# Optimization experiments

Measured on AMD Instinct MI355X. Metric: run time of the kernel, lower is better.

## Reference

```python
import jax, jax.numpy as jnp
import numpy as np

N_EXPERTS = 8
TOP_K = 2

def setup_inputs() -> dict:
    key = jax.random.key(0)
    k1, k2, k3, k4 = jax.random.split(key, 4)
    B, T, C, F, E = 4, 1024, 1024, 2048, N_EXPERTS
    x = jax.random.normal(k1, (B, T, C), dtype=jnp.float32)
    router_w = jax.random.normal(k2, (E, C), dtype=jnp.float32) * 0.02
    w_v = jax.random.normal(k3, (E, C, 2 * F), dtype=jnp.float32) * 0.02
    c_proj = jax.random.normal(k4, (E, F, C), dtype=jnp.float32) * 0.02
    return {"x": x, "router_w": router_w, "w_v": w_v, "c_proj": c_proj}

def reference(x, router_w, w_v, c_proj):
    B, T, C = x.shape
    E = router_w.shape[0]
    # Router: top-k softmax
    logits = jnp.einsum('btc,ec->bte', x, router_w)
    probs = jax.nn.softmax(logits, axis=-1)
    weights, indices = jax.lax.top_k(probs, TOP_K)          # [B,T,K]
    weights = weights / jnp.sum(weights, axis=-1, keepdims=True)
    avg_probs = jnp.mean(probs, axis=(0, 1))
    aux_loss = E * jnp.sum(avg_probs * avg_probs)
    # Dense per-expert SwiGLU MLP on all tokens (idiomatic jax MoE reference)
    xf = x.reshape(B * T, C)                                # [N,C]
    h = jnp.einsum('nc,ecf->enf', xf, w_v)                  # [E,N,2F]
    gate, value = jnp.split(h, 2, axis=-1)
    act = jax.nn.silu(gate) * value                         # [E,N,F]
    eo = jnp.einsum('enf,efc->nec', act, c_proj)            # [N,E,C]
    # Combine: gather each token's top-k expert outputs and weight-sum
    idx = indices.reshape(B * T, TOP_K)                     # [N,K]
    w = weights.reshape(B * T, TOP_K)                       # [N,K]
    sel = jnp.take_along_axis(eo, idx[:, :, None], axis=1)  # [N,K,C]
    out = jnp.sum(w[:, :, None] * sel, axis=1)              # [N,C]
    return out.reshape(B, T, C), aux_loss
```

## Files before the change

kernel.cpp:

```cpp
#include <hip/hip_runtime.h>
#include <hip/hip_bf16.h>
#include <stdint.h>

#define N_TOK 4096
#define C_DIM 1024
#define F_DIM 2048
#define E_NUM 8
#define SMAX 9216
#define TILES_MAX 72
#define RBLK 1024

typedef __attribute__((ext_vector_type(4))) float f32x4;
typedef __attribute__((ext_vector_type(8))) short s16x8;

__device__ __forceinline__ uint16_t f2bf(float f) {
    unsigned x;
    __builtin_memcpy(&x, &f, 4);
    unsigned r = (x + 0x7fffu + ((x >> 16) & 1u)) >> 16;
    return (uint16_t)r;
}
__device__ __forceinline__ float bf2f(uint16_t u) {
    unsigned v = (unsigned)u << 16;
    float f;
    __builtin_memcpy(&f, &v, 4);
    return f;
}

#define GLL16(gp, lp)                                                                  \
    __builtin_amdgcn_global_load_lds((const __attribute__((address_space(1))) unsigned int*)(gp), \
                                     (__attribute__((address_space(3))) unsigned int*)(lp), 16, 0, 0)

__global__ void router_kernel(const float* __restrict__ x, const float* __restrict__ rw,
                              int* __restrict__ topk_idx, float* __restrict__ topk_w,
                              float* __restrict__ psum_part, int* __restrict__ cnt_part) {
    __shared__ float s_p[E_NUM];
    __shared__ int s_c[E_NUM];
    if (threadIdx.x < E_NUM) { s_p[threadIdx.x] = 0.f; s_c[threadIdx.x] = 0; }
    __syncthreads();

    int lane = threadIdx.x & 63;
    int wv = threadIdx.x >> 6;
    int t = blockIdx.x * 4 + wv;

    const float* xr = x + (size_t)t * C_DIM + lane * 16;
    float xs[16];
    for (int i = 0; i < 4; i++) *(float4*)&xs[i * 4] = *(const float4*)(xr + i * 4);

    float acc[E_NUM];
    for (int e = 0; e < E_NUM; e++) {
        const float* wr = rw + e * C_DIM + lane * 16;
        float s = 0.f;
        for (int i = 0; i < 4; i++) {
            float4 v = *(const float4*)(wr + i * 4);
            s += xs[i * 4] * v.x + xs[i * 4 + 1] * v.y + xs[i * 4 + 2] * v.z + xs[i * 4 + 3] * v.w;
        }
        acc[e] = s;
    }
    for (int off = 32; off > 0; off >>= 1)
        for (int e = 0; e < E_NUM; e++) acc[e] += __shfl_down(acc[e], off, 64);

    if (lane == 0) {
        float m = acc[0];
        for (int e = 1; e < E_NUM; e++) m = fmaxf(m, acc[e]);
        float p[E_NUM], s = 0.f;
        for (int e = 0; e < E_NUM; e++) { p[e] = __expf(acc[e] - m); s += p[e]; }
        float inv = 1.f / s;
        for (int e = 0; e < E_NUM; e++) { p[e] *= inv; atomicAdd(&s_p[e], p[e]); }
        int i0 = 0;
        for (int e = 1; e < E_NUM; e++) if (p[e] > p[i0]) i0 = e;
        int i1 = (i0 == 0) ? 1 : 0;
        for (int e = 0; e < E_NUM; e++) if (e != i0 && p[e] > p[i1]) i1 = e;
        float w0 = p[i0], w1 = p[i1], wsum = w0 + w1;
        topk_idx[t * 2] = i0; topk_idx[t * 2 + 1] = i1;
        topk_w[t * 2] = w0 / wsum; topk_w[t * 2 + 1] = w1 / wsum;
        atomicAdd(&s_c[i0], 1); atomicAdd(&s_c[i1], 1);
    }
    __syncthreads();
    if (threadIdx.x < E_NUM) {
        psum_part[blockIdx.x * E_NUM + threadIdx.x] = s_p[threadIdx.x];
        cnt_part[blockIdx.x * E_NUM + threadIdx.x] = s_c[threadIdx.x];
    }
}

__global__ void reduce_plan_kernel(const float* __restrict__ psum_part, const int* __restrict__ cnt_part,
                                   int* __restrict__ offsets, int* __restrict__ tile_expert,
                                   int* __restrict__ tile_row0, float* __restrict__ aux_out) {
    __shared__ float sp[256];
    __shared__ int sc[256];
    __shared__ int s_count[E_NUM];
    __shared__ float s_psum[E_NUM];
    int e = threadIdx.x >> 5, i = threadIdx.x & 31;
    float fp = 0.f; int c = 0;
    for (int j = i; j < RBLK; j += 32) { fp += psum_part[j * E_NUM + e]; c += cnt_part[j * E_NUM + e]; }
    sp[threadIdx.x] = fp; sc[threadIdx.x] = c;
    __syncthreads();
    for (int s = 16; s > 0; s >>= 1) {
        if (i < s) { sp[threadIdx.x] += sp[threadIdx.x + s]; sc[threadIdx.x] += sc[threadIdx.x + s]; }
        __syncthreads();
    }
    if (i == 0) { s_count[e] = sc[threadIdx.x]; s_psum[e] = sp[threadIdx.x]; }
    __syncthreads();
    if (threadIdx.x == 0) {
        int off = 0, t = 0;
        for (int ee = 0; ee < E_NUM; ee++) {
            offsets[ee] = off;
            int n = s_count[ee];
            int nt = (n + 127) >> 7;
            for (int k = 0; k < nt; k++) { tile_expert[t] = ee; tile_row0[t] = off + k * 128; t++; }
            off += nt * 128;
        }
        offsets[E_NUM] = off;
        for (; t < TILES_MAX; t++) tile_expert[t] = -1;
        float s = 0.f;
        for (int ee = 0; ee < E_NUM; ee++) { float a = s_psum[ee] * (1.f / N_TOK); s += a * a; }
        aux_out[0] = 8.f * s;
    }
}

__global__ void assign_kernel(const int* __restrict__ topk_idx, const float* __restrict__ topk_w,
                              const int* __restrict__ offsets, int* __restrict__ count2,
                              int* __restrict__ slot_map, float* __restrict__ slot_w,
                              int* __restrict__ tok_slot) {
    __shared__ int h[E_NUM];
    __shared__ int base[E_NUM];
    if (threadIdx.x < E_NUM) h[threadIdx.x] = 0;
    __syncthreads();
    int item = blockIdx.x * 256 + threadIdx.x;
    int e = topk_idx[item];
    int rank = atomicAdd(&h[e], 1);
    __syncthreads();
    if (threadIdx.x < E_NUM)
        base[threadIdx.x] = offsets[threadIdx.x] + atomicAdd(&count2[threadIdx.x], h[threadIdx.x]);
    __syncthreads();
    int slot = base[e] + rank;
    slot_map[slot] = item;
    slot_w[slot] = topk_w[item];
    tok_slot[item] = slot;
}

__global__ void gather_kernel(const float* __restrict__ x, const int* __restrict__ slot_map,
                              uint16_t* __restrict__ x_slots) {
    int slot = blockIdx.x;
    int item = slot_map[slot];
    if (item < 0) return;
    int t = item >> 1;
    float4 v = *(const float4*)(x + (size_t)t * C_DIM + threadIdx.x * 4);
    union { uint16_t u[4]; uint2 q; } r;
    r.u[0] = f2bf(v.x); r.u[1] = f2bf(v.y); r.u[2] = f2bf(v.z); r.u[3] = f2bf(v.w);
    *(uint2*)(x_slots + (size_t)slot * C_DIM + threadIdx.x * 4) = r.q;
}

__global__ __launch_bounds__(256) void convT_kernel(const float* __restrict__ in,
                                                    uint16_t* __restrict__ out, int R, int Cc) {
    __shared__ uint16_t s[128 * 66];
    size_t zb = (size_t)blockIdx.z * (size_t)R * Cc;
    int c0 = blockIdx.x * 64, r0 = blockIdx.y * 128;
    int cx = (threadIdx.x & 15) * 4, ry = threadIdx.x >> 4;
    for (int j = 0; j < 8; j++) {
        int r = ry + j * 16;
        float4 v = *(const float4*)(in + zb + (size_t)(r0 + r) * Cc + c0 + cx);
        uint16_t* p = &s[r * 66 + cx];
        p[0] = f2bf(v.x); p[1] = f2bf(v.y); p[2] = f2bf(v.z); p[3] = f2bf(v.w);
    }
    __syncthreads();
    int oc = threadIdx.x & 63, wseg = threadIdx.x >> 6;
    uint16_t tmp[32];
    for (int j = 0; j < 32; j++) tmp[j] = s[(wseg * 32 + j) * 66 + oc];
    uint4* dst = (uint4*)(out + zb + (size_t)(c0 + oc) * R + r0 + wseg * 32);
    dst[0] = *(const uint4*)&tmp[0];
    dst[1] = *(const uint4*)&tmp[8];
    dst[2] = *(const uint4*)&tmp[16];
    dst[3] = *(const uint4*)&tmp[24];
}


__global__ __launch_bounds__(256) void gemm1_kernel(const uint16_t* __restrict__ x_slots,
                                                    const uint16_t* __restrict__ wvT,
                                                    const int* __restrict__ tile_expert,
                                                    const int* __restrict__ tile_row0,
                                                    uint16_t* __restrict__ act) {
    int e = tile_expert[blockIdx.y];
    if (e < 0) return;
    int row0 = tile_row0[blockIdx.y];
    int j = blockIdx.x;
    __shared__ uint16_t As[128 * 32];
    __shared__ uint16_t Bg[64 * 32];
    __shared__ uint16_t Bv[64 * 32];
    int lane = threadIdx.x & 63, w = threadIdx.x >> 6;
    int wm = w & 1, wn = w >> 1;
    const uint16_t* wvb = wvT + (size_t)e * 4096 * 1024;

    int sk = (((lane & 3) ^ ((lane >> 3) & 3))) * 8;
    int ar = w * 32 + (lane >> 2);
    const uint16_t* agp0 = x_slots + (size_t)(row0 + ar) * C_DIM + sk;
    const uint16_t* agp1 = agp0 + (size_t)16 * C_DIM;
    int br = w * 16 + (lane >> 2);
    const uint16_t* bgp = wvb + (size_t)(j * 64 + br) * C_DIM + sk;
    const uint16_t* bvp = wvb + (size_t)(2048 + j * 64 + br) * C_DIM + sk;

    int cswz = ((lane >> 4) ^ ((lane >> 1) & 3)) * 8;

    f32x4 accg[4][2], accv[4][2];
    f32x4 z4 = {0.f, 0.f, 0.f, 0.f};
    for (int mf = 0; mf < 4; mf++)
        for (int nf = 0; nf < 2; nf++) { accg[mf][nf] = z4; accv[mf][nf] = z4; }

    for (int kt = 0; kt < 32; ++kt) {
        int ko = kt * 32;
        __syncthreads();
        GLL16(agp0 + ko, As + w * 1024);
        GLL16(agp1 + ko, As + w * 1024 + 512);
        GLL16(bgp + ko, Bg + w * 512);
        GLL16(bvp + ko, Bv + w * 512);
        __syncthreads();
        s16x8 af[4], bg[2], bv[2];
        for (int mf = 0; mf < 4; mf++)
            af[mf] = *(const s16x8*)&As[(wm * 64 + mf * 16 + (lane & 15)) * 32 + cswz];
        for (int nf = 0; nf < 2; nf++) {
            bg[nf] = *(const s16x8*)&Bg[(wn * 32 + nf * 16 + (lane & 15)) * 32 + cswz];
            bv[nf] = *(const s16x8*)&Bv[(wn * 32 + nf * 16 + (lane & 15)) * 32 + cswz];
        }
        for (int mf = 0; mf < 4; mf++)
            for (int nf = 0; nf < 2; nf++) {
                accg[mf][nf] = __builtin_amdgcn_mfma_f32_16x16x32_bf16(af[mf], bg[nf], accg[mf][nf], 0, 0, 0);
                accv[mf][nf] = __builtin_amdgcn_mfma_f32_16x16x32_bf16(af[mf], bv[nf], accv[mf][nf], 0, 0, 0);
            }
    }
    for (int mf = 0; mf < 4; mf++)
        for (int nf = 0; nf < 2; nf++)
            for (int r = 0; r < 4; r++) {
                int row = row0 + wm * 64 + mf * 16 + (lane >> 4) * 4 + r;
                int col = j * 64 + wn * 32 + nf * 16 + (lane & 15);
                float g = accg[mf][nf][r], v = accv[mf][nf][r];
                float a = g * v / (1.f + __expf(-g));
                act[(size_t)row * F_DIM + col] = f2bf(a);
            }
}

__global__ __launch_bounds__(256) void gemm2_kernel(const uint16_t* __restrict__ act,
                                                    const uint16_t* __restrict__ cpT,
                                                    const int* __restrict__ tile_expert,
                                                    const int* __restrict__ tile_row0,
                                                    const int* __restrict__ slot_map,
                                                    const float* __restrict__ slot_w,
                                                    uint16_t* __restrict__ eo) {
    int e = tile_expert[blockIdx.y];
    if (e < 0) return;
    int row0 = tile_row0[blockIdx.y];
    int cb = blockIdx.x * 128;
    __shared__ uint16_t As[128 * 32];
    __shared__ uint16_t Bs[128 * 32];
    int lane = threadIdx.x & 63, w = threadIdx.x >> 6;
    int wm = w & 1, wn = w >> 1;
    const uint16_t* cpb = cpT + (size_t)e * 1024 * 2048;

    int sk = (((lane & 3) ^ ((lane >> 3) & 3))) * 8;
    int ar = w * 32 + (lane >> 2);
    const uint16_t* agp0 = act + (size_t)(row0 + ar) * F_DIM + sk;
    const uint16_t* agp1 = agp0 + (size_t)16 * F_DIM;
    const uint16_t* bgp0 = cpb + (size_t)(cb + ar) * F_DIM + sk;
    const uint16_t* bgp1 = bgp0 + (size_t)16 * F_DIM;

    int cswz = ((lane >> 4) ^ ((lane >> 1) & 3)) * 8;

    f32x4 acc[4][4];
    f32x4 z4 = {0.f, 0.f, 0.f, 0.f};
    for (int mf = 0; mf < 4; mf++)
        for (int nf = 0; nf < 4; nf++) acc[mf][nf] = z4;

    for (int kt = 0; kt < 64; ++kt) {
        int ko = kt * 32;
        __syncthreads();
        GLL16(agp0 + ko, As + w * 1024);
        GLL16(agp1 + ko, As + w * 1024 + 512);
        GLL16(bgp0 + ko, Bs + w * 1024);
        GLL16(bgp1 + ko, Bs + w * 1024 + 512);
        __syncthreads();
        s16x8 af[4], bf[4];
        for (int mf = 0; mf < 4; mf++)
            af[mf] = *(const s16x8*)&As[(wm * 64 + mf * 16 + (lane & 15)) * 32 + cswz];
        for (int nf = 0; nf < 4; nf++)
            bf[nf] = *(const s16x8*)&Bs[(wn * 64 + nf * 16 + (lane & 15)) * 32 + cswz];
        for (int mf = 0; mf < 4; mf++)
            for (int nf = 0; nf < 4; nf++)
                acc[mf][nf] = __builtin_amdgcn_mfma_f32_16x16x32_bf16(af[mf], bf[nf], acc[mf][nf], 0, 0, 0);
    }
    for (int mf = 0; mf < 4; mf++)
        for (int r = 0; r < 4; r++) {
            int slotr = row0 + wm * 64 + mf * 16 + (lane >> 4) * 4 + r;
            int t2k = slot_map[slotr];
            if (t2k < 0) continue;
            float wgt = slot_w[slotr];
            for (int nf = 0; nf < 4; nf++) {
                int col = cb + wn * 64 + nf * 16 + (lane & 15);
                eo[(size_t)slotr * C_DIM + col] = f2bf(wgt * acc[mf][nf][r]);
            }
        }
}

__global__ void combine_kernel(const uint16_t* __restrict__ eo, const int* __restrict__ tok_slot,
                               float* __restrict__ out) {
    int t = blockIdx.x;
    int s0 = tok_slot[2 * t], s1 = tok_slot[2 * t + 1];
    int c = threadIdx.x * 4;
    uint2 a = *(const uint2*)(eo + (size_t)s0 * C_DIM + c);
    uint2 b = *(const uint2*)(eo + (size_t)s1 * C_DIM + c);
    float4 o;
    o.x = bf2f((uint16_t)(a.x & 0xffff)) + bf2f((uint16_t)(b.x & 0xffff));
    o.y = bf2f((uint16_t)(a.x >> 16)) + bf2f((uint16_t)(b.x >> 16));
    o.z = bf2f((uint16_t)(a.y & 0xffff)) + bf2f((uint16_t)(b.y & 0xffff));
    o.w = bf2f((uint16_t)(a.y >> 16)) + bf2f((uint16_t)(b.y >> 16));
    *(float4*)(out + (size_t)t * C_DIM + c) = o;
}

extern "C" void kernel_launch(void* const* d_in, const int* in_sizes, int n_in,
                              void* d_out, int out_size, void* d_ws, size_t ws_size,
                              hipStream_t stream) {
    (void)in_sizes; (void)n_in; (void)out_size; (void)ws_size;
    const float* x = (const float*)d_in[0];
    const float* rw = (const float*)d_in[1];
    const float* wv = (const float*)d_in[2];
    const float* cp = (const float*)d_in[3];
    float* out = (float*)d_out;

    char* ws = (char*)d_ws;
    size_t off = 0;
    auto alloc = [&](size_t sz) -> void* {
        off = (off + 255) & ~(size_t)255;
        void* p = ws + off;
        off += sz;
        return p;
    };
    uint16_t* wvT = (uint16_t*)alloc((size_t)E_NUM * 4096 * 1024 * 2);
    uint16_t* cpT = (uint16_t*)alloc((size_t)E_NUM * 1024 * 2048 * 2);
    uint16_t* x_slots = (uint16_t*)alloc((size_t)SMAX * C_DIM * 2);
    uint16_t* act = (uint16_t*)alloc((size_t)SMAX * F_DIM * 2);
    uint16_t* eo = (uint16_t*)alloc((size_t)SMAX * C_DIM * 2);
    float* psum_part = (float*)alloc((size_t)RBLK * E_NUM * 4);
    int* cnt_part = (int*)alloc((size_t)RBLK * E_NUM * 4);
    int* count2 = (int*)alloc(E_NUM * 4);
    int* offsets = (int*)alloc((E_NUM + 1) * 4);
    int* tile_expert = (int*)alloc(TILES_MAX * 4);
    int* tile_row0 = (int*)alloc(TILES_MAX * 4);
    int* topk_idx = (int*)alloc((size_t)N_TOK * 2 * 4);
    float* topk_w = (float*)alloc((size_t)N_TOK * 2 * 4);
    int* slot_map = (int*)alloc((size_t)SMAX * 4);
    float* slot_w = (float*)alloc((size_t)SMAX * 4);
    int* tok_slot = (int*)alloc((size_t)N_TOK * 2 * 4);

    hipMemsetAsync(count2, 0, E_NUM * 4, stream);
    hipMemsetAsync(slot_map, 0xFF, (size_t)SMAX * 4, stream);

    router_kernel<<<RBLK, 256, 0, stream>>>(x, rw, topk_idx, topk_w, psum_part, cnt_part);
    reduce_plan_kernel<<<1, 256, 0, stream>>>(psum_part, cnt_part, offsets, tile_expert, tile_row0,
                                              out + (size_t)N_TOK * C_DIM);
    assign_kernel<<<N_TOK * 2 / 256, 256, 0, stream>>>(topk_idx, topk_w, offsets, count2,
                                                       slot_map, slot_w, tok_slot);
    gather_kernel<<<SMAX, 256, 0, stream>>>(x, slot_map, x_slots);
    convT_kernel<<<dim3(4096 / 64, 1024 / 128, E_NUM), 256, 0, stream>>>(wv, wvT, 1024, 4096);
    convT_kernel<<<dim3(1024 / 64, 2048 / 128, E_NUM), 256, 0, stream>>>(cp, cpT, 2048, 1024);
    gemm1_kernel<<<dim3(32, TILES_MAX), 256, 0, stream>>>(x_slots, wvT, tile_expert, tile_row0, act);
    gemm2_kernel<<<dim3(8, TILES_MAX), 256, 0, stream>>>(act, cpT, tile_expert, tile_row0,
                                                         slot_map, slot_w, eo);
    combine_kernel<<<N_TOK, 256, 0, stream>>>(eo, tok_slot, out);
}
```

Before: 483.4 us.

## Double-buffer LDS in grouped GEMMs and swap grid axes for tile order

Both expert GEMM kernels now keep two LDS buffers, so the global-to-LDS loads for the next K-step are issued before the MFMA work on the current step, and one barrier per iteration is removed. The grid axes are also swapped so that consecutive blocks walk over token tiles that share the same weight column block, which changes L2 reuse of the weights. LDS use per block doubles, which may lower occupancy.

After: 518.1 us. +7.2%, slower.

```diff
diff --git a/kernel.cpp b/kernel.cpp
--- a/kernel.cpp
+++ b/kernel.cpp
@@ -179,13 +179,13 @@
                                                     const int* __restrict__ tile_expert,
                                                     const int* __restrict__ tile_row0,
                                                     uint16_t* __restrict__ act) {
-    int e = tile_expert[blockIdx.y];
+    int e = tile_expert[blockIdx.x];
     if (e < 0) return;
-    int row0 = tile_row0[blockIdx.y];
-    int j = blockIdx.x;
-    __shared__ uint16_t As[128 * 32];
-    __shared__ uint16_t Bg[64 * 32];
-    __shared__ uint16_t Bv[64 * 32];
+    int row0 = tile_row0[blockIdx.x];
+    int j = blockIdx.y;
+    __shared__ uint16_t As[2][128 * 32];
+    __shared__ uint16_t Bg[2][64 * 32];
+    __shared__ uint16_t Bv[2][64 * 32];
     int lane = threadIdx.x & 63, w = threadIdx.x >> 6;
     int wm = w & 1, wn = w >> 1;
     const uint16_t* wvb = wvT + (size_t)e * 4096 * 1024;
@@ -205,27 +205,41 @@
     for (int mf = 0; mf < 4; mf++)
         for (int nf = 0; nf < 2; nf++) { accg[mf][nf] = z4; accv[mf][nf] = z4; }
 
-    for (int kt = 0; kt < 32; ++kt) {
-        int ko = kt * 32;
+#define G1_STAGE(b, ko)                               \
+    do {                                              \
+        GLL16(agp0 + (ko), &As[b][w * 1024]);         \
+        GLL16(agp1 + (ko), &As[b][w * 1024 + 512]);   \
+        GLL16(bgp + (ko), &Bg[b][w * 512]);           \
+        GLL16(bvp + (ko), &Bv[b][w * 512]);           \
+    } while (0)
+
+#define G1_COMPUTE(b)                                                                           \
+    do {                                                                                        \
+        s16x8 af[4], bg[2], bv[2];                                                              \
+        for (int mf = 0; mf < 4; mf++)                                                          \
+            af[mf] = *(const s16x8*)&As[b][(wm * 64 + mf * 16 + (lane & 15)) * 32 + cswz];      \
+        for (int nf = 0; nf < 2; nf++) {                                                        \
+            bg[nf] = *(const s16x8*)&Bg[b][(wn * 32 + nf * 16 + (lane & 15)) * 32 + cswz];      \
+            bv[nf] = *(const s16x8*)&Bv[b][(wn * 32 + nf * 16 + (lane & 15)) * 32 + cswz];      \
+        }                                                                                       \
+        for (int mf = 0; mf < 4; mf++)                                                          \
+            for (int nf = 0; nf < 2; nf++) {                                                    \
+                accg[mf][nf] = __builtin_amdgcn_mfma_f32_16x16x32_bf16(af[mf], bg[nf], accg[mf][nf], 0, 0, 0); \
+                accv[mf][nf] = __builtin_amdgcn_mfma_f32_16x16x32_bf16(af[mf], bv[nf], accv[mf][nf], 0, 0, 0); \
+            }                                                                                   \
+    } while (0)
+
+    G1_STAGE(0, 0);
+    __syncthreads();
+    int cur = 0;
+    for (int kt = 0; kt < 31; ++kt) {
+        G1_STAGE(cur ^ 1, (kt + 1) * 32);
+        G1_COMPUTE(cur);
         __syncthreads();
-        GLL16(agp0 + ko, As + w * 1024);
-        GLL16(agp1 + ko, As + w * 1024 + 512);
-        GLL16(bgp + ko, Bg + w * 512);
-        GLL16(bvp + ko, Bv + w * 512);
-        __syncthreads();
-        s16x8 af[4], bg[2], bv[2];
-        for (int mf = 0; mf < 4; mf++)
-            af[mf] = *(const s16x8*)&As[(wm * 64 + mf * 16 + (lane & 15)) * 32 + cswz];
-        for (int nf = 0; nf < 2; nf++) {
-            bg[nf] = *(const s16x8*)&Bg[(wn * 32 + nf * 16 + (lane & 15)) * 32 + cswz];
-            bv[nf] = *(const s16x8*)&Bv[(wn * 32 + nf * 16 + (lane & 15)) * 32 + cswz];
-        }
-        for (int mf = 0; mf < 4; mf++)
-            for (int nf = 0; nf < 2; nf++) {
-                accg[mf][nf] = __builtin_amdgcn_mfma_f32_16x16x32_bf16(af[mf], bg[nf], accg[mf][nf], 0, 0, 0);
-                accv[mf][nf] = __builtin_amdgcn_mfma_f32_16x16x32_bf16(af[mf], bv[nf], accv[mf][nf], 0, 0, 0);
-            }
-    }
+        cur ^= 1;
+    }
+    G1_COMPUTE(cur);
+
     for (int mf = 0; mf < 4; mf++)
         for (int nf = 0; nf < 2; nf++)
             for (int r = 0; r < 4; r++) {
@@ -244,12 +258,12 @@
                                                     const int* __restrict__ slot_map,
                                                     const float* __restrict__ slot_w,
                                                     uint16_t* __restrict__ eo) {
-    int e = tile_expert[blockIdx.y];
+    int e = tile_expert[blockIdx.x];
     if (e < 0) return;
-    int row0 = tile_row0[blockIdx.y];
-    int cb = blockIdx.x * 128;
-    __shared__ uint16_t As[128 * 32];
-    __shared__ uint16_t Bs[128 * 32];
+    int row0 = tile_row0[blockIdx.x];
+    int cb = blockIdx.y * 128;
+    __shared__ uint16_t As[2][128 * 32];
+    __shared__ uint16_t Bs[2][128 * 32];
     int lane = threadIdx.x & 63, w = threadIdx.x >> 6;
     int wm = w & 1, wn = w >> 1;
     const uint16_t* cpb = cpT + (size_t)e * 1024 * 2048;
@@ -268,23 +282,37 @@
     for (int mf = 0; mf < 4; mf++)
         for (int nf = 0; nf < 4; nf++) acc[mf][nf] = z4;
 
-    for (int kt = 0; kt < 64; ++kt) {
-        int ko = kt * 32;
+#define G2_STAGE(b, ko)                               \
+    do {                                              \
+        GLL16(agp0 + (ko), &As[b][w * 1024]);         \
+        GLL16(agp1 + (ko), &As[b][w * 1024 + 512]);   \
+        GLL16(bgp0 + (ko), &Bs[b][w * 1024]);         \
+        GLL16(bgp1 + (ko), &Bs[b][w * 1024 + 512]);   \
+    } while (0)
+
+#define G2_COMPUTE(b)                                                                           \
+    do {                                                                                        \
+        s16x8 af[4], bf[4];                                                                     \
+        for (int mf = 0; mf < 4; mf++)                                                          \
+            af[mf] = *(const s16x8*)&As[b][(wm * 64 + mf * 16 + (lane & 15)) * 32 + cswz];      \
+        for (int nf = 0; nf < 4; nf++)                                                          \
+            bf[nf] = *(const s16x8*)&Bs[b][(wn * 64 + nf * 16 + (lane & 15)) * 32 + cswz];      \
+        for (int mf = 0; mf < 4; mf++)                                                          \
+            for (int nf = 0; nf < 4; nf++)                                                      \
+                acc[mf][nf] = __builtin_amdgcn_mfma_f32_16x16x32_bf16(af[mf], bf[nf], acc[mf][nf], 0, 0, 0); \
+    } while (0)
+
+    G2_STAGE(0, 0);
+    __syncthreads();
+    int cur = 0;
+    for (int kt = 0; kt < 63; ++kt) {
+        G2_STAGE(cur ^ 1, (kt + 1) * 32);
+        G2_COMPUTE(cur);
         __syncthreads();
-        GLL16(agp0 + ko, As + w * 1024);
-        GLL16(agp1 + ko, As + w * 1024 + 512);
-        GLL16(bgp0 + ko, Bs + w * 1024);
-        GLL16(bgp1 + ko, Bs + w * 1024 + 512);
-        __syncthreads();
-        s16x8 af[4], bf[4];
-        for (int mf = 0; mf < 4; mf++)
-            af[mf] = *(const s16x8*)&As[(wm * 64 + mf * 16 + (lane & 15)) * 32 + cswz];
-        for (int nf = 0; nf < 4; nf++)
-            bf[nf] = *(const s16x8*)&Bs[(wn * 64 + nf * 16 + (lane & 15)) * 32 + cswz];
-        for (int mf = 0; mf < 4; mf++)
-            for (int nf = 0; nf < 4; nf++)
-                acc[mf][nf] = __builtin_amdgcn_mfma_f32_16x16x32_bf16(af[mf], bf[nf], acc[mf][nf], 0, 0, 0);
-    }
+        cur ^= 1;
+    }
+    G2_COMPUTE(cur);
+
     for (int mf = 0; mf < 4; mf++)
         for (int r = 0; r < 4; r++) {
             int slotr = row0 + wm * 64 + mf * 16 + (lane >> 4) * 4 + r;
@@ -359,8 +387,8 @@
     gather_kernel<<<SMAX, 256, 0, stream>>>(x, slot_map, x_slots);
     convT_kernel<<<dim3(4096 / 64, 1024 / 128, E_NUM), 256, 0, stream>>>(wv, wvT, 1024, 4096);
     convT_kernel<<<dim3(1024 / 64, 2048 / 128, E_NUM), 256, 0, stream>>>(cp, cpT, 2048, 1024);
-    gemm1_kernel<<<dim3(32, TILES_MAX), 256, 0, stream>>>(x_slots, wvT, tile_expert, tile_row0, act);
-    gemm2_kernel<<<dim3(8, TILES_MAX), 256, 0, stream>>>(act, cpT, tile_expert, tile_row0,
+    gemm1_kernel<<<dim3(TILES_MAX, 32), 256, 0, stream>>>(x_slots, wvT, tile_expert, tile_row0, act);
+    gemm2_kernel<<<dim3(TILES_MAX, 8), 256, 0, stream>>>(act, cpT, tile_expert, tile_row0,
                                                          slot_map, slot_w, eo);
     combine_kernel<<<N_TOK, 256, 0, stream>>>(eo, tok_slot, out);
 }
```

## Rewrite gemm1 as 256x256 tile with pipelined LDS staging and interleaved weights

Applied to the files above, without the earlier changes.

Replaces the 128x64 gate/value gemm1 with a 512-thread, 256x256 tile kernel. It uses a 128KB LDS double buffer, issues loads asynchronously with explicit vmcnt waits and barriers, raises wave priority around the MFMA blocks, and swizzles block IDs. The wv transpose now interleaves gate and value rows in 16-row blocks so a single B tile feeds both products. Routing pads experts to 256-row tiles with a separate 128-row plan for gemm2, and eo reuses the x_slots buffer. The aim is more data reuse and better latency hiding in the main GEMM. The cost is larger padding (SMAX grows), heavy LDS use that limits occupancy, and fragile hand-written synchronisation.

Measured after the change: 486.8 us. No clear change (+0.7%).

```diff
diff --git a/kernel.cpp b/kernel.cpp
--- a/kernel.cpp
+++ b/kernel.cpp
@@ -6,8 +6,9 @@
 #define C_DIM 1024
 #define F_DIM 2048
 #define E_NUM 8
-#define SMAX 9216
-#define TILES_MAX 72
+#define SMAX 10240
+#define T256_MAX 40
+#define T128_MAX 72
 #define RBLK 1024
 
 typedef __attribute__((ext_vector_type(4))) float f32x4;
@@ -83,8 +84,9 @@
 }
 
 __global__ void reduce_plan_kernel(const float* __restrict__ psum_part, const int* __restrict__ cnt_part,
-                                   int* __restrict__ offsets, int* __restrict__ tile_expert,
-                                   int* __restrict__ tile_row0, float* __restrict__ aux_out) {
+                                   int* __restrict__ offsets, int* __restrict__ tile_e256,
+                                   int* __restrict__ tile_r256, int* __restrict__ tile_e128,
+                                   int* __restrict__ tile_r128, float* __restrict__ aux_out) {
     __shared__ float sp[256];
     __shared__ int sc[256];
     __shared__ int s_count[E_NUM];
@@ -101,16 +103,19 @@
     if (i == 0) { s_count[e] = sc[threadIdx.x]; s_psum[e] = sp[threadIdx.x]; }
     __syncthreads();
     if (threadIdx.x == 0) {
-        int off = 0, t = 0;
+        int off = 0, t2 = 0, t1 = 0;
         for (int ee = 0; ee < E_NUM; ee++) {
             offsets[ee] = off;
             int n = s_count[ee];
-            int nt = (n + 127) >> 7;
-            for (int k = 0; k < nt; k++) { tile_expert[t] = ee; tile_row0[t] = off + k * 128; t++; }
-            off += nt * 128;
+            int nt2 = (n + 255) >> 8;
+            for (int k = 0; k < nt2; k++) { tile_e256[t2] = ee; tile_r256[t2] = off + k * 256; t2++; }
+            int nt1 = (n + 127) >> 7;
+            for (int k = 0; k < nt1; k++) { tile_e128[t1] = ee; tile_r128[t1] = off + k * 128; t1++; }
+            off += nt2 * 256;
         }
         offsets[E_NUM] = off;
-        for (; t < TILES_MAX; t++) tile_expert[t] = -1;
+        for (; t2 < T256_MAX; t2++) tile_e256[t2] = -1;
+        for (; t1 < T128_MAX; t1++) tile_e128[t1] = -1;
         float s = 0.f;
         for (int ee = 0; ee < E_NUM; ee++) { float a = s_psum[ee] * (1.f / N_TOK); s += a * a; }
         aux_out[0] = 8.f * s;
@@ -151,7 +156,8 @@
 }
 
 __global__ __launch_bounds__(256) void convT_kernel(const float* __restrict__ in,
-                                                    uint16_t* __restrict__ out, int R, int Cc) {
+                                                    uint16_t* __restrict__ out, int R, int Cc,
+                                                    int remap) {
     __shared__ uint16_t s[128 * 66];
     size_t zb = (size_t)blockIdx.z * (size_t)R * Cc;
     int c0 = blockIdx.x * 64, r0 = blockIdx.y * 128;
@@ -166,7 +172,13 @@
     int oc = threadIdx.x & 63, wseg = threadIdx.x >> 6;
     uint16_t tmp[32];
     for (int j = 0; j < 32; j++) tmp[j] = s[(wseg * 32 + j) * 66 + oc];
-    uint4* dst = (uint4*)(out + zb + (size_t)(c0 + oc) * R + r0 + wseg * 32);
+    int orow = c0 + oc;
+    if (remap) {
+        int b = orow >> 4;
+        int nb = (b < 128) ? (b * 2) : ((b - 128) * 2 + 1);
+        orow = nb * 16 + (orow & 15);
+    }
+    uint4* dst = (uint4*)(out + zb + (size_t)orow * R + r0 + wseg * 32);
     dst[0] = *(const uint4*)&tmp[0];
     dst[1] = *(const uint4*)&tmp[8];
     dst[2] = *(const uint4*)&tmp[16];
@@ -174,79 +186,124 @@
 }
 
 
-__global__ __launch_bounds__(256) void gemm1_kernel(const uint16_t* __restrict__ x_slots,
-                                                    const uint16_t* __restrict__ wvT,
-                                                    const int* __restrict__ tile_expert,
-                                                    const int* __restrict__ tile_row0,
-                                                    uint16_t* __restrict__ act) {
-    int e = tile_expert[blockIdx.y];
+#define A_OFF(b, h) (((b) * 2 + (h)) * 8192)
+#define B_OFF(b, h) (32768 + ((b) * 2 + (h)) * 8192)
+
+__global__ __launch_bounds__(512, 2) void gemm1_kernel(const uint16_t* __restrict__ x_slots,
+                                                       const uint16_t* __restrict__ wvT,
+                                                       const int* __restrict__ tile_e256,
+                                                       const int* __restrict__ tile_r256,
+                                                       uint16_t* __restrict__ act) {
+    __shared__ uint16_t LDS[65536];
+    int bid = blockIdx.x;
+    int swz = (bid & 7) * 80 + (bid >> 3);
+    int my = swz >> 4, j = swz & 15;
+    int e = tile_e256[my];
     if (e < 0) return;
-    int row0 = tile_row0[blockIdx.y];
-    int j = blockIdx.x;
-    __shared__ uint16_t As[128 * 32];
-    __shared__ uint16_t Bg[64 * 32];
-    __shared__ uint16_t Bv[64 * 32];
-    int lane = threadIdx.x & 63, w = threadIdx.x >> 6;
-    int wm = w & 1, wn = w >> 1;
+    int row0 = tile_r256[my];
+    int lane = threadIdx.x & 63, v = threadIdx.x >> 6;
+    int wm = v & 1, wn = v >> 1;
     const uint16_t* wvb = wvT + (size_t)e * 4096 * 1024;
 
-    int sk = (((lane & 3) ^ ((lane >> 3) & 3))) * 8;
-    int ar = w * 32 + (lane >> 2);
-    const uint16_t* agp0 = x_slots + (size_t)(row0 + ar) * C_DIM + sk;
-    const uint16_t* agp1 = agp0 + (size_t)16 * C_DIM;
-    int br = w * 16 + (lane >> 2);
-    const uint16_t* bgp = wvb + (size_t)(j * 64 + br) * C_DIM + sk;
-    const uint16_t* bvp = wvb + (size_t)(2048 + j * 64 + br) * C_DIM + sk;
-
+    int sk = ((lane & 3) ^ ((lane >> 3) & 3)) * 8;
+    int srow = v * 32 + (lane >> 2);
+    const uint16_t* aSrc0 = x_slots + (size_t)(row0 + srow) * C_DIM + sk;
+    const uint16_t* aSrc1 = aSrc0 + (size_t)16 * C_DIM;
+    const uint16_t* bSrc0 = wvb + (size_t)(j * 256 + srow) * C_DIM + sk;
+    const uint16_t* bSrc1 = bSrc0 + (size_t)16 * C_DIM;
     int cswz = ((lane >> 4) ^ ((lane >> 1) & 3)) * 8;
 
-    f32x4 accg[4][2], accv[4][2];
+    f32x4 acc[8][4];
     f32x4 z4 = {0.f, 0.f, 0.f, 0.f};
-    for (int mf = 0; mf < 4; mf++)
-        for (int nf = 0; nf < 2; nf++) { accg[mf][nf] = z4; accv[mf][nf] = z4; }
-
-    for (int kt = 0; kt < 32; ++kt) {
-        int ko = kt * 32;
-        __syncthreads();
-        GLL16(agp0 + ko, As + w * 1024);
-        GLL16(agp1 + ko, As + w * 1024 + 512);
-        GLL16(bgp + ko, Bg + w * 512);
-        GLL16(bvp + ko, Bv + w * 512);
-        __syncthreads();
-        s16x8 af[4], bg[2], bv[2];
-        for (int mf = 0; mf < 4; mf++)
-            af[mf] = *(const s16x8*)&As[(wm * 64 + mf * 16 + (lane & 15)) * 32 + cswz];
-        for (int nf = 0; nf < 2; nf++) {
-            bg[nf] = *(const s16x8*)&Bg[(wn * 32 + nf * 16 + (lane & 15)) * 32 + cswz];
-            bv[nf] = *(const s16x8*)&Bv[(wn * 32 + nf * 16 + (lane & 15)) * 32 + cswz];
+#pragma unroll
+    for (int m = 0; m < 8; m++)
+#pragma unroll
+        for (int n = 0; n < 4; n++) acc[m][n] = z4;
+    s16x8 bfr[4];
+
+#define STAGE_A(b, h, ko)                                              \
+    do {                                                               \
+        GLL16(aSrc0 + (ko) + (h) * 32, &LDS[A_OFF(b, h) + v * 1024]);  \
+        GLL16(aSrc1 + (ko) + (h) * 32, &LDS[A_OFF(b, h) + v * 1024 + 512]); \
+    } while (0)
+#define STAGE_B(b, h, ko)                                              \
+    do {                                                               \
+        GLL16(bSrc0 + (ko) + (h) * 32, &LDS[B_OFF(b, h) + v * 1024]);  \
+        GLL16(bSrc1 + (ko) + (h) * 32, &LDS[B_OFF(b, h) + v * 1024 + 512]); \
+    } while (0)
+
+#define PHASE(b, kh, mh, LB, STG, WEND)                                                        \
+    do {                                                                                       \
+        s16x8 af[4];                                                                           \
+        _Pragma("unroll") for (int mf = 0; mf < 4; mf++)                                       \
+            af[mf] = *(const s16x8*)&LDS[A_OFF(b, kh) +                                        \
+                     (wm * 128 + ((mh) * 4 + mf) * 16 + (lane & 15)) * 32 + cswz];             \
+        if (LB) {                                                                              \
+            _Pragma("unroll") for (int nf = 0; nf < 4; nf++)                                   \
+                bfr[nf] = *(const s16x8*)&LDS[B_OFF(b, kh) +                                   \
+                          (wn * 64 + nf * 16 + (lane & 15)) * 32 + cswz];                      \
+        }                                                                                      \
+        STG;                                                                                   \
+        asm volatile("s_barrier" ::: "memory");                                                \
+        __builtin_amdgcn_s_setprio(1);                                                         \
+        _Pragma("unroll") for (int mf = 0; mf < 4; mf++)                                       \
+            _Pragma("unroll") for (int nf = 0; nf < 4; nf++)                                   \
+                acc[(mh) * 4 + mf][nf] = __builtin_amdgcn_mfma_f32_16x16x32_bf16(              \
+                    af[mf], bfr[nf], acc[(mh) * 4 + mf][nf], 0, 0, 0);                         \
+        __builtin_amdgcn_s_setprio(0);                                                         \
+        if (WEND) asm volatile("s_waitcnt vmcnt(8)" ::: "memory");                             \
+        asm volatile("s_barrier" ::: "memory");                                                \
+    } while (0)
+
+    asm volatile("s_waitcnt vmcnt(0) lgkmcnt(0)" ::: "memory");
+    STAGE_A(0, 0, 0); STAGE_B(0, 0, 0);
+    STAGE_A(0, 1, 0); STAGE_B(0, 1, 0);
+    STAGE_A(1, 0, 64); STAGE_B(1, 0, 64);
+    asm volatile("s_waitcnt vmcnt(8)" ::: "memory");
+    asm volatile("s_barrier" ::: "memory");
+
+    for (int i = 0; i < 8; i++) {
+        int ko1 = ((2 * i + 1) & 15) * 64;
+        int ko2 = ((2 * i + 2) & 15) * 64;
+        int ko3 = ((2 * i + 3) & 15) * 64;
+        PHASE(0, 0, 0, 1, STAGE_A(1, 1, ko1), 0);
+        PHASE(0, 0, 1, 0, STAGE_B(1, 1, ko1), 1);
+        PHASE(0, 1, 0, 1, STAGE_A(0, 0, ko2), 0);
+        PHASE(0, 1, 1, 0, STAGE_B(0, 0, ko2), 1);
+        PHASE(1, 0, 0, 1, STAGE_A(0, 1, ko2), 0);
+        PHASE(1, 0, 1, 0, STAGE_B(0, 1, ko2), 1);
+        PHASE(1, 1, 0, 1, STAGE_A(1, 0, ko3), 0);
+        PHASE(1, 1, 1, 0, STAGE_B(1, 0, ko3), 1);
+    }
+
+#pragma unroll
+    for (int mfa = 0; mfa < 8; mfa++)
+#pragma unroll
+        for (int nfp = 0; nfp < 2; nfp++) {
+            f32x4 g = acc[mfa][nfp * 2], vv = acc[mfa][nfp * 2 + 1];
+#pragma unroll
+            for (int r = 0; r < 4; r++) {
+                int row = row0 + wm * 128 + mfa * 16 + (lane >> 4) * 4 + r;
+                int f = j * 128 + wn * 32 + nfp * 16 + (lane & 15);
+                float a = g[r] * vv[r] / (1.f + __expf(-g[r]));
+                act[(size_t)row * F_DIM + f] = f2bf(a);
+            }
         }
-        for (int mf = 0; mf < 4; mf++)
-            for (int nf = 0; nf < 2; nf++) {
-                accg[mf][nf] = __builtin_amdgcn_mfma_f32_16x16x32_bf16(af[mf], bg[nf], accg[mf][nf], 0, 0, 0);
-                accv[mf][nf] = __builtin_amdgcn_mfma_f32_16x16x32_bf16(af[mf], bv[nf], accv[mf][nf], 0, 0, 0);
-            }
-    }
-    for (int mf = 0; mf < 4; mf++)
-        for (int nf = 0; nf < 2; nf++)
-            for (int r = 0; r < 4; r++) {
-                int row = row0 + wm * 64 + mf * 16 + (lane >> 4) * 4 + r;
-                int col = j * 64 + wn * 32 + nf * 16 + (lane & 15);
-                float g = accg[mf][nf][r], v = accv[mf][nf][r];
-                float a = g * v / (1.f + __expf(-g));
-                act[(size_t)row * F_DIM + col] = f2bf(a);
-            }
+#undef STAGE_A
+#undef STAGE_B
+#undef PHASE
 }
 
 __global__ __launch_bounds__(256) void gemm2_kernel(const uint16_t* __restrict__ act,
                                                     const uint16_t* __restrict__ cpT,
-                                                    const int* __restrict__ tile_expert,
-                                                    const int* __restrict__ tile_row0,
+                                                    const int* __restrict__ tile_e128,
+                                                    const int* __restrict__ tile_r128,
                                                     const int* __restrict__ slot_map,
                                                     const float* __restrict__ slot_w,
                                                     uint16_t* __restrict__ eo) {
-    int e = tile_expert[blockIdx.y];
+    int e = tile_e128[blockIdx.y];
     if (e < 0) return;
-    int row0 = tile_row0[blockIdx.y];
+    int row0 = tile_r128[blockIdx.y];
     int cb = blockIdx.x * 128;
     __shared__ uint16_t As[128 * 32];
     __shared__ uint16_t Bs[128 * 32];
@@ -335,13 +392,15 @@
     uint16_t* cpT = (uint16_t*)alloc((size_t)E_NUM * 1024 * 2048 * 2);
     uint16_t* x_slots = (uint16_t*)alloc((size_t)SMAX * C_DIM * 2);
     uint16_t* act = (uint16_t*)alloc((size_t)SMAX * F_DIM * 2);
-    uint16_t* eo = (uint16_t*)alloc((size_t)SMAX * C_DIM * 2);
+    uint16_t* eo = x_slots;
     float* psum_part = (float*)alloc((size_t)RBLK * E_NUM * 4);
     int* cnt_part = (int*)alloc((size_t)RBLK * E_NUM * 4);
     int* count2 = (int*)alloc(E_NUM * 4);
     int* offsets = (int*)alloc((E_NUM + 1) * 4);
-    int* tile_expert = (int*)alloc(TILES_MAX * 4);
-    int* tile_row0 = (int*)alloc(TILES_MAX * 4);
+    int* tile_e256 = (int*)alloc(T256_MAX * 4);
+    int* tile_r256 = (int*)alloc(T256_MAX * 4);
+    int* tile_e128 = (int*)alloc(T128_MAX * 4);
+    int* tile_r128 = (int*)alloc(T128_MAX * 4);
     int* topk_idx = (int*)alloc((size_t)N_TOK * 2 * 4);
     float* topk_w = (float*)alloc((size_t)N_TOK * 2 * 4);
     int* slot_map = (int*)alloc((size_t)SMAX * 4);
@@ -352,15 +411,15 @@
     hipMemsetAsync(slot_map, 0xFF, (size_t)SMAX * 4, stream);
 
     router_kernel<<<RBLK, 256, 0, stream>>>(x, rw, topk_idx, topk_w, psum_part, cnt_part);
-    reduce_plan_kernel<<<1, 256, 0, stream>>>(psum_part, cnt_part, offsets, tile_expert, tile_row0,
-                                              out + (size_t)N_TOK * C_DIM);
+    reduce_plan_kernel<<<1, 256, 0, stream>>>(psum_part, cnt_part, offsets, tile_e256, tile_r256,
+                                              tile_e128, tile_r128, out + (size_t)N_TOK * C_DIM);
     assign_kernel<<<N_TOK * 2 / 256, 256, 0, stream>>>(topk_idx, topk_w, offsets, count2,
                                                        slot_map, slot_w, tok_slot);
     gather_kernel<<<SMAX, 256, 0, stream>>>(x, slot_map, x_slots);
-    convT_kernel<<<dim3(4096 / 64, 1024 / 128, E_NUM), 256, 0, stream>>>(wv, wvT, 1024, 4096);
-    convT_kernel<<<dim3(1024 / 64, 2048 / 128, E_NUM), 256, 0, stream>>>(cp, cpT, 2048, 1024);
-    gemm1_kernel<<<dim3(32, TILES_MAX), 256, 0, stream>>>(x_slots, wvT, tile_expert, tile_row0, act);
-    gemm2_kernel<<<dim3(8, TILES_MAX), 256, 0, stream>>>(act, cpT, tile_expert, tile_row0,
-                                                         slot_map, slot_w, eo);
+    convT_kernel<<<dim3(4096 / 64, 1024 / 128, E_NUM), 256, 0, stream>>>(wv, wvT, 1024, 4096, 1);
+    convT_kernel<<<dim3(1024 / 64, 2048 / 128, E_NUM), 256, 0, stream>>>(cp, cpT, 2048, 1024, 0);
+    gemm1_kernel<<<16 * T256_MAX, 512, 0, stream>>>(x_slots, wvT, tile_e256, tile_r256, act);
+    gemm2_kernel<<<dim3(8, T128_MAX), 256, 0, stream>>>(act, cpT, tile_e128, tile_r128,
+                                                        slot_map, slot_w, eo);
     combine_kernel<<<N_TOK, 256, 0, stream>>>(eo, tok_slot, out);
 }
```
